# Performance work log

Measured on AMD Instinct MI355X. Metric: run time of the kernel, lower is better.

The kernel has to match this reference:

```python
import jax, jax.numpy as jnp
import numpy as np

N_INP = 512
N_HID = 512
BATCH = 64
STEPS = 512


def setup_inputs() -> dict:
    key = jax.random.key(0)
    ks = jax.random.split(key, 7)

    def xavier(k, n_in, n_out):
        bound = np.sqrt(3.0) * np.sqrt(2.0 / float(n_in + n_out))
        return jax.random.uniform(k, (n_in, n_out), jnp.float32, -bound, bound)

    return {
        "inputs": jax.random.normal(ks[0], (BATCH, STEPS, N_INP), jnp.float32),
        "W_xz": xavier(ks[1], N_INP, N_HID),
        "W_hz": xavier(ks[2], N_HID, N_HID),
        "b_z": jnp.zeros((N_HID,), jnp.float32),
        "W_xr": xavier(ks[3], N_INP, N_HID),
        "W_hr": xavier(ks[4], N_HID, N_HID),
        "b_r": jnp.zeros((N_HID,), jnp.float32),
        "W_xh": xavier(ks[5], N_INP, N_HID),
        "W_hh": xavier(ks[6], N_HID, N_HID),
        "b_h": jnp.zeros((N_HID,), jnp.float32),
        "train": 0,
    }


def reference(inputs, W_xz, W_hz, b_z, W_xr, W_hr, b_r, W_xh, W_hh, b_h, train):
    # inputs: (B, T, n_inp). GRU with eval-mode (dropout_rate=0), so the
    # dropout branch in the original forward is a no-op.
    B = inputs.shape[0]
    H0 = jnp.zeros((B, W_hz.shape[0]), inputs.dtype)

    def step(H_t, X_t):
        Z_t = jax.nn.sigmoid(X_t @ W_xz + H_t @ W_hz + b_z)
        R_t = jax.nn.sigmoid(X_t @ W_xr + H_t @ W_hr + b_r)
        H_tilde = jnp.tanh(X_t @ W_xh + (R_t * H_t) @ W_hh + b_h)
        H_new = Z_t * H_t + (1.0 - Z_t) * H_tilde
        return H_new, H_new

    xs = jnp.swapaxes(inputs, 0, 1)  # (T, B, n_inp)
    H_final, outs = jax.lax.scan(step, H0, xs)
    outputs = jnp.swapaxes(outs, 0, 1)  # (B, T, n_hid)
    return outputs, H_final
```

## Files before the change

### kernel.cpp

```cpp
#include <hip/hip_runtime.h>

#define B_   64
#define T_   512
#define KIN  512
#define NH   512
#define KEFF 3072
#define NBLK 64
#define NTHR 256

typedef __attribute__((ext_vector_type(8))) short short8;
typedef __attribute__((ext_vector_type(4))) float f32x4;
typedef __attribute__((ext_vector_type(4))) unsigned int u32x4;

__device__ __forceinline__ unsigned short f2b(float f) {
    union { float f; unsigned int u; } v; v.f = f;
    unsigned int u = v.u;
    return (unsigned short)((u + 0x7FFFu + ((u >> 16) & 1u)) >> 16);
}
__device__ __forceinline__ float b2f(unsigned short h) {
    union { float f; unsigned int u; } v; v.u = ((unsigned int)h) << 16;
    return v.f;
}

__global__ void prepack(const float* __restrict__ Wxz, const float* __restrict__ Whz,
                        const float* __restrict__ Wxr, const float* __restrict__ Whr,
                        const float* __restrict__ Wxh, const float* __restrict__ Whh,
                        unsigned short* __restrict__ Bzr, unsigned short* __restrict__ Bh) {
    int keff = blockIdx.x * 256 + threadIdx.x;
    int n    = blockIdx.y;
    int seg  = keff >> 9;
    int k    = keff & 511;
    const float* src;
    int c;
    if (n < 512)       { c = n;        src = (seg < 3) ? Whz : Wxz; }
    else if (n < 1024) { c = n - 512;  src = (seg < 3) ? Whr : Wxr; }
    else               { c = n - 1024; src = (seg < 3) ? Whh : Wxh; }
    float w = src[k * NH + c];
    unsigned short hi = f2b(w);
    unsigned short o  = (seg == 2 || seg == 5) ? f2b(w - b2f(hi)) : hi;
    if (n < 1024) Bzr[(size_t)n * KEFF + keff] = o;
    else          Bh[(size_t)(n - 1024) * KEFF + keff] = o;
}

__device__ __forceinline__ unsigned int ald32(const unsigned int* p) {
    return __hip_atomic_load(p, __ATOMIC_RELAXED, __HIP_MEMORY_SCOPE_AGENT);
}
__device__ __forceinline__ unsigned long long ald64(const void* p) {
    return __hip_atomic_load((const unsigned long long*)p, __ATOMIC_RELAXED,
                             __HIP_MEMORY_SCOPE_AGENT);
}
__device__ __forceinline__ void ast32(unsigned int* p, unsigned int v) {
    __hip_atomic_store(p, v, __ATOMIC_RELAXED, __HIP_MEMORY_SCOPE_AGENT);
}
__device__ __forceinline__ void ast64(void* p, unsigned long long v) {
    __hip_atomic_store((unsigned long long*)p, v, __ATOMIC_RELAXED,
                       __HIP_MEMORY_SCOPE_AGENT);
}

__device__ __forceinline__ void flag_wait(const unsigned int* flags,
                                          unsigned int tgt, int lane) {
    while (1) {
        unsigned int v = ald32(flags + lane);
        if (__all((int)(v >= tgt))) break;
    }
    __builtin_amdgcn_sched_barrier(0);
}

__device__ __forceinline__ int hp_idx(int m, int c) {
    return m * 512 + (c ^ ((m & 7) << 2));
}

__device__ __forceinline__ void cvt_x8(const float* xr, int kp, short8* ahi, short8* alo) {
    f32x4 x0 = *(const f32x4*)(xr + kp);
    f32x4 x1 = *(const f32x4*)(xr + kp + 4);
#pragma unroll
    for (int i = 0; i < 4; ++i) {
        unsigned short h0 = f2b(x0[i]);
        (*ahi)[i] = (short)h0; (*alo)[i] = (short)f2b(x0[i] - b2f(h0));
        unsigned short h1 = f2b(x1[i]);
        (*ahi)[4 + i] = (short)h1; (*alo)[4 + i] = (short)f2b(x1[i] - b2f(h1));
    }
}

__device__ __forceinline__ void unpackw(u32x4 w0, u32x4 w1, short8* ahi, short8* alo) {
    union { unsigned int u[4]; short8 v; } H, L;
    H.u[0] = __builtin_amdgcn_perm(w0[1], w0[0], 0x05040100u);
    H.u[1] = __builtin_amdgcn_perm(w0[3], w0[2], 0x05040100u);
    H.u[2] = __builtin_amdgcn_perm(w1[1], w1[0], 0x05040100u);
    H.u[3] = __builtin_amdgcn_perm(w1[3], w1[2], 0x05040100u);
    L.u[0] = __builtin_amdgcn_perm(w0[1], w0[0], 0x07060302u);
    L.u[1] = __builtin_amdgcn_perm(w0[3], w0[2], 0x07060302u);
    L.u[2] = __builtin_amdgcn_perm(w1[1], w1[0], 0x07060302u);
    L.u[3] = __builtin_amdgcn_perm(w1[3], w1[2], 0x07060302u);
    *ahi = H.v; *alo = L.v;
}

#define MFMA(a, b, c) __builtin_amdgcn_mfma_f32_16x16x32_bf16((a), (b), (c), 0, 0, 0)

__global__ void __launch_bounds__(NTHR, 1) gru_seq(
    const float* __restrict__ X, const float* __restrict__ bz,
    const float* __restrict__ br, const float* __restrict__ bh,
    float* __restrict__ out, float* __restrict__ Zt,
    unsigned int* __restrict__ HP, unsigned int* __restrict__ RHP,
    const unsigned short* __restrict__ Bzr, const unsigned short* __restrict__ Bh,
    unsigned int* flags) {
    const int blk  = blockIdx.x;
    const int tid  = threadIdx.x;
    const int wv   = tid >> 6;
    const int lane = tid & 63;
    const int fm   = lane & 15;
    const int fkc  = lane >> 4;
    const int fk   = fkc * 8;

    __shared__ unsigned int hbuf[4 * 16 * 512];
    __shared__ float comb[2][256];

    const int m1 = wv * 16 + fm;
    const unsigned short* Bp1 = Bzr + (size_t)(blk * 16 + fm) * KEFF;
    const int c1 = blk * 16 + fm;

    const int mt    = blk & 3;
    const int slot  = wv >> 1;
    const int khalf = wv & 1;
    const int nt    = (blk >> 2) * 2 + slot;
    const int m2    = mt * 16 + fm;
    const unsigned short* Bp2 = Bh + (size_t)(nt * 16 + fm) * KEFF;
    const int c2 = nt * 16 + fm;

    const int key = (fm & 7) << 4;
    const int sw0 = (32 * fkc) ^ key;
    const int sw1 = (32 * fkc + 16) ^ key;

    const char* HPb  = (const char*)HP;
    const char* RHPb = (const char*)RHP;

    for (int t = 0; t < T_; ++t) {
        const unsigned int ep = (unsigned int)t * 2u;
        {
            f32x4 acc = {0.f, 0.f, 0.f, 0.f};
            const float* xr = X + (size_t)m1 * (T_ * KIN) + (size_t)t * KIN;
#pragma unroll 4
            for (int j = 0; j < 16; ++j) {
                int kp = j * 32 + fk;
                short8 xhi, xlo; cvt_x8(xr, kp, &xhi, &xlo);
                short8 b3 = *(const short8*)(Bp1 + 1536 + kp);
                short8 b4 = *(const short8*)(Bp1 + 2048 + kp);
                short8 b5 = *(const short8*)(Bp1 + 2560 + kp);
                acc = MFMA(xhi, b3, acc); acc = MFMA(xlo, b4, acc); acc = MFMA(xhi, b5, acc);
            }
            if (wv == 0 && t) flag_wait(flags, ep, lane);
            __syncthreads();
            {
                const char* src = HPb + wv * 32768;
                char* dst = (char*)hbuf + wv * 32768;
#pragma unroll
                for (int i = 0; i < 32; ++i)
                    __builtin_amdgcn_global_load_lds(
                        (const unsigned int*)(src + i * 1024 + lane * 16),
                        (unsigned int*)(dst + i * 1024), 16, 0, 0x11);
            }
            asm volatile("s_waitcnt vmcnt(0)" ::: "memory");
            __builtin_amdgcn_sched_barrier(0);
            {
                const char* sl = (const char*)hbuf + wv * 32768 + fm * 2048;
#pragma unroll 4
                for (int j = 0; j < 16; ++j) {
                    u32x4 w0 = *(const u32x4*)(sl + 128 * j + sw0);
                    u32x4 w1 = *(const u32x4*)(sl + 128 * j + sw1);
                    short8 ahi, alo; unpackw(w0, w1, &ahi, &alo);
                    int kp = j * 32 + fk;
                    short8 b0 = *(const short8*)(Bp1 + kp);
                    short8 b1 = *(const short8*)(Bp1 + 512 + kp);
                    short8 b2 = *(const short8*)(Bp1 + 1024 + kp);
                    acc = MFMA(ahi, b0, acc); acc = MFMA(alo, b1, acc); acc = MFMA(ahi, b2, acc);
                }
            }
            if (blk < 32) {
                float bzi = bz[c1];
                float g[4];
#pragma unroll
                for (int jj = 0; jj < 4; ++jj)
                    g[jj] = 1.f / (1.f + __expf(-(acc[jj] + bzi)));
                union { float f[2]; unsigned long long q; } p0, p1;
                p0.f[0] = g[0]; p0.f[1] = g[1];
                p1.f[0] = g[2]; p1.f[1] = g[3];
                float* zp = Zt + c1 * 64 + wv * 16 + fkc * 4;
                ast64(zp, p0.q); ast64(zp + 2, p1.q);
            } else {
                int cr = c1 - 512;
                float bri = br[cr];
#pragma unroll
                for (int jj = 0; jj < 4; ++jj) {
                    int lr = fkc * 4 + jj;
                    unsigned int hw = *(const unsigned int*)((const char*)hbuf +
                        wv * 32768 + lr * 2048 + ((4 * cr) ^ ((lr & 7) << 4)));
                    float h  = b2f((unsigned short)(hw & 0xffffu)) +
                               b2f((unsigned short)(hw >> 16));
                    float gr = 1.f / (1.f + __expf(-(acc[jj] + bri)));
                    float rh = gr * h;
                    unsigned short hi = f2b(rh);
                    unsigned short lo = f2b(rh - b2f(hi));
                    ast32(RHP + hp_idx(wv * 16 + lr, cr),
                          (unsigned int)hi | ((unsigned int)lo << 16));
                }
            }
        }
        __syncthreads();
        if (tid == 0) ast32(flags + blk, ep + 1u);
        {
            f32x4 acc2 = {0.f, 0.f, 0.f, 0.f};
            if (khalf == 1) {
                const float* xr = X + (size_t)m2 * (T_ * KIN) + (size_t)t * KIN;
#pragma unroll 4
                for (int j = 0; j < 16; ++j) {
                    int kp = j * 32 + fk;
                    short8 xhi, xlo; cvt_x8(xr, kp, &xhi, &xlo);
                    short8 b3 = *(const short8*)(Bp2 + 1536 + kp);
                    short8 b4 = *(const short8*)(Bp2 + 2048 + kp);
                    short8 b5 = *(const short8*)(Bp2 + 2560 + kp);
                    acc2 = MFMA(xhi, b3, acc2); acc2 = MFMA(xlo, b4, acc2); acc2 = MFMA(xhi, b5, acc2);
                }
#pragma unroll
                for (int jj = 0; jj < 4; ++jj)
                    comb[slot][(fkc * 4 + jj) * 16 + fm] = acc2[jj];
            }
            if (wv == 0) flag_wait(flags, ep + 1u, lane);
            __syncthreads();
            unsigned long long zq0 = 0, zq1 = 0;
            if (khalf == 0) {
                const float* zp = Zt + c2 * 64 + mt * 16 + fkc * 4;
                zq0 = ald64(zp); zq1 = ald64(zp + 2);
            }
            {
                const char* src = RHPb + mt * 32768;
                char* dst = (char*)hbuf + ((mt + 2) & 3) * 32768;
#pragma unroll
                for (int i = 0; i < 8; ++i) {
                    int o = (wv * 8 + i) * 1024;
                    __builtin_amdgcn_global_load_lds(
                        (const unsigned int*)(src + o + lane * 16),
                        (unsigned int*)(dst + o), 16, 0, 0x11);
                }
            }
            asm volatile("s_waitcnt vmcnt(0)" ::: "memory");
            __builtin_amdgcn_sched_barrier(0);
            __syncthreads();
            if (khalf == 0) {
                const char* sl = (const char*)hbuf + ((mt + 2) & 3) * 32768 + fm * 2048;
#pragma unroll 4
                for (int j = 0; j < 16; ++j) {
                    u32x4 w0 = *(const u32x4*)(sl + 128 * j + sw0);
                    u32x4 w1 = *(const u32x4*)(sl + 128 * j + sw1);
                    short8 ahi, alo; unpackw(w0, w1, &ahi, &alo);
                    int kp = j * 32 + fk;
                    short8 b0 = *(const short8*)(Bp2 + kp);
                    short8 b1 = *(const short8*)(Bp2 + 512 + kp);
                    short8 b2 = *(const short8*)(Bp2 + 1024 + kp);
                    acc2 = MFMA(ahi, b0, acc2); acc2 = MFMA(alo, b1, acc2); acc2 = MFMA(ahi, b2, acc2);
                }
                union { unsigned long long q; float f[2]; } z0, z1;
                z0.q = zq0; z1.q = zq1;
                float zv[4] = {z0.f[0], z0.f[1], z1.f[0], z1.f[1]};
                float bhi = bh[c2];
#pragma unroll
                for (int jj = 0; jj < 4; ++jj) {
                    int lr   = fkc * 4 + jj;
                    int mrow = mt * 16 + lr;
                    unsigned int hw = *(const unsigned int*)((const char*)hbuf +
                        mt * 32768 + lr * 2048 + ((4 * c2) ^ ((lr & 7) << 4)));
                    float h   = b2f((unsigned short)(hw & 0xffffu)) +
                                b2f((unsigned short)(hw >> 16));
                    float pre = acc2[jj] + comb[slot][lr * 16 + fm] + bhi;
                    float e   = __expf(-2.f * pre);
                    float ht  = 2.f / (1.f + e) - 1.f;
                    float hn  = zv[jj] * h + (1.f - zv[jj]) * ht;
                    out[(size_t)mrow * (T_ * NH) + (size_t)t * NH + c2] = hn;
                    if (t == T_ - 1)
                        out[(size_t)B_ * T_ * NH + mrow * NH + c2] = hn;
                    unsigned short hi = f2b(hn);
                    unsigned short lo = f2b(hn - b2f(hi));
                    ast32(HP + hp_idx(mrow, c2),
                          (unsigned int)hi | ((unsigned int)lo << 16));
                }
            }
        }
        __syncthreads();
        if (tid == 0) ast32(flags + blk, ep + 2u);
    }
}

extern "C" void kernel_launch(void* const* d_in, const int* in_sizes, int n_in,
                              void* d_out, int out_size, void* d_ws, size_t ws_size,
                              hipStream_t stream) {
    (void)in_sizes; (void)n_in; (void)out_size; (void)ws_size;
    const float* X   = (const float*)d_in[0];
    const float* Wxz = (const float*)d_in[1];
    const float* Whz = (const float*)d_in[2];
    const float* bz  = (const float*)d_in[3];
    const float* Wxr = (const float*)d_in[4];
    const float* Whr = (const float*)d_in[5];
    const float* br  = (const float*)d_in[6];
    const float* Wxh = (const float*)d_in[7];
    const float* Whh = (const float*)d_in[8];
    const float* bh  = (const float*)d_in[9];
    float* out = (float*)d_out;

    char* ws = (char*)d_ws;
    unsigned int* flags = (unsigned int*)ws;
    float* Zt         = (float*)(ws + 256);
    unsigned int* HP  = (unsigned int*)(ws + 256 + 131072);
    unsigned int* RHP = (unsigned int*)(ws + 256 + 262144);
    unsigned short* Bzr = (unsigned short*)(ws + (1 << 20));
    unsigned short* Bh  = Bzr + (size_t)1024 * KEFF;

    hipMemsetAsync(d_ws, 0, 1 << 20, stream);
    prepack<<<dim3(12, 1536), 256, 0, stream>>>(Wxz, Whz, Wxr, Whr, Wxh, Whh, Bzr, Bh);
    gru_seq<<<NBLK, NTHR, 0, stream>>>(X, bz, br, bh, out, Zt, HP, RHP, Bzr, Bh, flags);
}
```

Before: 14.78 ms.

## Add producer warps that precompute next-step input projections, split recurrent K

Doubles the block to 512 threads. Four extra waves (an "x crew") compute the input-side projections X·W for step t+1 into double-buffered shared memory. Meanwhile the original four waves do the recurrent H·W products and gates for step t, which takes the input GEMM off the serial critical path. The candidate-state recurrent matmul is also split across two waves per tile by K halves and combined through shared memory. The cost is more shared memory, extra barriers, and higher register and wave pressure per CU.

```diff
diff --git a/kernel.cpp b/kernel.cpp
--- a/kernel.cpp
+++ b/kernel.cpp
@@ -6,7 +6,7 @@
 #define NH   512
 #define KEFF 3072
 #define NBLK 64
-#define NTHR 256
+#define NTHR 512
 
 typedef __attribute__((ext_vector_type(8))) short short8;
 typedef __attribute__((ext_vector_type(4))) float f32x4;
@@ -97,7 +97,7 @@
 
 #define MFMA(a, b, c) __builtin_amdgcn_mfma_f32_16x16x32_bf16((a), (b), (c), 0, 0, 0)
 
-__global__ void __launch_bounds__(NTHR, 1) gru_seq(
+__global__ void __launch_bounds__(NTHR, 2) gru_seq(
     const float* __restrict__ X, const float* __restrict__ bz,
     const float* __restrict__ br, const float* __restrict__ bh,
     float* __restrict__ out, float* __restrict__ Zt,
@@ -107,181 +107,204 @@
     const int blk  = blockIdx.x;
     const int tid  = threadIdx.x;
     const int wv   = tid >> 6;
+    const int hwv  = wv & 3;
+    const bool xcrew = wv >= 4;
     const int lane = tid & 63;
     const int fm   = lane & 15;
     const int fkc  = lane >> 4;
     const int fk   = fkc * 8;
 
     __shared__ unsigned int hbuf[4 * 16 * 512];
+    __shared__ float xp1[2][4][16][16];
+    __shared__ float xp2a[2][2][16][16];
+    __shared__ float xp2b[2][2][16][16];
     __shared__ float comb[2][256];
 
-    const int m1 = wv * 16 + fm;
+    const int m1 = hwv * 16 + fm;
     const unsigned short* Bp1 = Bzr + (size_t)(blk * 16 + fm) * KEFF;
     const int c1 = blk * 16 + fm;
 
-    const int mt    = blk & 3;
-    const int slot  = wv >> 1;
-    const int khalf = wv & 1;
-    const int nt    = (blk >> 2) * 2 + slot;
-    const int m2    = mt * 16 + fm;
+    const int mt  = blk & 3;
+    const int s2i = hwv >> 1;
+    const int jh  = hwv & 1;
+    const int nt  = (blk >> 2) * 2 + s2i;
+    const int m2  = mt * 16 + fm;
     const unsigned short* Bp2 = Bh + (size_t)(nt * 16 + fm) * KEFF;
     const int c2 = nt * 16 + fm;
 
     const int key = (fm & 7) << 4;
     const int sw0 = (32 * fkc) ^ key;
     const int sw1 = (32 * fkc + 16) ^ key;
-
     const char* HPb  = (const char*)HP;
     const char* RHPb = (const char*)RHP;
 
+    const float bias1 = (blk < 32) ? bz[c1] : br[c1 - 512];
+    const float bhi   = bh[c2];
+
+    auto xg1 = [&](int tt, int buf) {
+        f32x4 acc = {0.f, 0.f, 0.f, 0.f};
+        const float* xr = X + (size_t)m1 * (T_ * KIN) + (size_t)tt * KIN;
+#pragma unroll 4
+        for (int j = 0; j < 16; ++j) {
+            int kp = j * 32 + fk;
+            short8 xhi, xlo; cvt_x8(xr, kp, &xhi, &xlo);
+            short8 b3 = *(const short8*)(Bp1 + 1536 + kp);
+            short8 b4 = *(const short8*)(Bp1 + 2048 + kp);
+            short8 b5 = *(const short8*)(Bp1 + 2560 + kp);
+            acc = MFMA(xhi, b3, acc); acc = MFMA(xlo, b4, acc); acc = MFMA(xhi, b5, acc);
+        }
+#pragma unroll
+        for (int jj = 0; jj < 4; ++jj) xp1[buf][hwv][fkc * 4 + jj][fm] = acc[jj];
+    };
+    auto xg2 = [&](int tt, int buf) {
+        f32x4 acc = {0.f, 0.f, 0.f, 0.f};
+        const float* xr = X + (size_t)m2 * (T_ * KIN) + (size_t)tt * KIN;
+#pragma unroll
+        for (int j = jh * 8; j < jh * 8 + 8; ++j) {
+            int kp = j * 32 + fk;
+            short8 xhi, xlo; cvt_x8(xr, kp, &xhi, &xlo);
+            short8 b3 = *(const short8*)(Bp2 + 1536 + kp);
+            short8 b4 = *(const short8*)(Bp2 + 2048 + kp);
+            short8 b5 = *(const short8*)(Bp2 + 2560 + kp);
+            acc = MFMA(xhi, b3, acc); acc = MFMA(xlo, b4, acc); acc = MFMA(xhi, b5, acc);
+        }
+        float (*dst)[16][16] = jh ? xp2b[buf] : xp2a[buf];
+#pragma unroll
+        for (int jj = 0; jj < 4; ++jj) dst[s2i][fkc * 4 + jj][fm] = acc[jj];
+    };
+
+    if (xcrew) { xg1(0, 0); xg2(0, 0); }
+    __syncthreads();
+
     for (int t = 0; t < T_; ++t) {
+        const int bufc = t & 1, bufn = bufc ^ 1;
         const unsigned int ep = (unsigned int)t * 2u;
-        {
+        if (wv == 0 && t) flag_wait(flags, ep, lane);
+        __syncthreads();
+        if (!xcrew) {
+            const char* src = HPb + hwv * 32768;
+            char* dst = (char*)hbuf + hwv * 32768;
+#pragma unroll
+            for (int i = 0; i < 32; ++i)
+                __builtin_amdgcn_global_load_lds(
+                    (const unsigned int*)(src + i * 1024 + lane * 16),
+                    (unsigned int*)(dst + i * 1024), 16, 0, 0x11);
+            asm volatile("s_waitcnt vmcnt(0)" ::: "memory");
+            __builtin_amdgcn_sched_barrier(0);
             f32x4 acc = {0.f, 0.f, 0.f, 0.f};
-            const float* xr = X + (size_t)m1 * (T_ * KIN) + (size_t)t * KIN;
+            const char* sl = (const char*)hbuf + hwv * 32768 + fm * 2048;
 #pragma unroll 4
             for (int j = 0; j < 16; ++j) {
+                u32x4 w0 = *(const u32x4*)(sl + 128 * j + sw0);
+                u32x4 w1 = *(const u32x4*)(sl + 128 * j + sw1);
+                short8 ahi, alo; unpackw(w0, w1, &ahi, &alo);
                 int kp = j * 32 + fk;
-                short8 xhi, xlo; cvt_x8(xr, kp, &xhi, &xlo);
-                short8 b3 = *(const short8*)(Bp1 + 1536 + kp);
-                short8 b4 = *(const short8*)(Bp1 + 2048 + kp);
-                short8 b5 = *(const short8*)(Bp1 + 2560 + kp);
-                acc = MFMA(xhi, b3, acc); acc = MFMA(xlo, b4, acc); acc = MFMA(xhi, b5, acc);
-            }
-            if (wv == 0 && t) flag_wait(flags, ep, lane);
-            __syncthreads();
-            {
-                const char* src = HPb + wv * 32768;
-                char* dst = (char*)hbuf + wv * 32768;
-#pragma unroll
-                for (int i = 0; i < 32; ++i)
-                    __builtin_amdgcn_global_load_lds(
-                        (const unsigned int*)(src + i * 1024 + lane * 16),
-                        (unsigned int*)(dst + i * 1024), 16, 0, 0x11);
-            }
-            asm volatile("s_waitcnt vmcnt(0)" ::: "memory");
-            __builtin_amdgcn_sched_barrier(0);
-            {
-                const char* sl = (const char*)hbuf + wv * 32768 + fm * 2048;
-#pragma unroll 4
-                for (int j = 0; j < 16; ++j) {
-                    u32x4 w0 = *(const u32x4*)(sl + 128 * j + sw0);
-                    u32x4 w1 = *(const u32x4*)(sl + 128 * j + sw1);
-                    short8 ahi, alo; unpackw(w0, w1, &ahi, &alo);
-                    int kp = j * 32 + fk;
-                    short8 b0 = *(const short8*)(Bp1 + kp);
-                    short8 b1 = *(const short8*)(Bp1 + 512 + kp);
-                    short8 b2 = *(const short8*)(Bp1 + 1024 + kp);
-                    acc = MFMA(ahi, b0, acc); acc = MFMA(alo, b1, acc); acc = MFMA(ahi, b2, acc);
-                }
+                short8 b0 = *(const short8*)(Bp1 + kp);
+                short8 b1 = *(const short8*)(Bp1 + 512 + kp);
+                short8 b2 = *(const short8*)(Bp1 + 1024 + kp);
+                acc = MFMA(ahi, b0, acc); acc = MFMA(alo, b1, acc); acc = MFMA(ahi, b2, acc);
             }
             if (blk < 32) {
-                float bzi = bz[c1];
                 float g[4];
 #pragma unroll
                 for (int jj = 0; jj < 4; ++jj)
-                    g[jj] = 1.f / (1.f + __expf(-(acc[jj] + bzi)));
+                    g[jj] = 1.f / (1.f + __expf(-(acc[jj] +
+                              xp1[bufc][hwv][fkc * 4 + jj][fm] + bias1)));
                 union { float f[2]; unsigned long long q; } p0, p1;
                 p0.f[0] = g[0]; p0.f[1] = g[1];
                 p1.f[0] = g[2]; p1.f[1] = g[3];
-                float* zp = Zt + c1 * 64 + wv * 16 + fkc * 4;
+                float* zp = Zt + c1 * 64 + hwv * 16 + fkc * 4;
                 ast64(zp, p0.q); ast64(zp + 2, p1.q);
             } else {
                 int cr = c1 - 512;
-                float bri = br[cr];
 #pragma unroll
                 for (int jj = 0; jj < 4; ++jj) {
                     int lr = fkc * 4 + jj;
                     unsigned int hw = *(const unsigned int*)((const char*)hbuf +
-                        wv * 32768 + lr * 2048 + ((4 * cr) ^ ((lr & 7) << 4)));
+                        hwv * 32768 + lr * 2048 + ((4 * cr) ^ ((lr & 7) << 4)));
                     float h  = b2f((unsigned short)(hw & 0xffffu)) +
                                b2f((unsigned short)(hw >> 16));
-                    float gr = 1.f / (1.f + __expf(-(acc[jj] + bri)));
+                    float gr = 1.f / (1.f + __expf(-(acc[jj] +
+                                 xp1[bufc][hwv][lr][fm] + bias1)));
                     float rh = gr * h;
                     unsigned short hi = f2b(rh);
                     unsigned short lo = f2b(rh - b2f(hi));
-                    ast32(RHP + hp_idx(wv * 16 + lr, cr),
+                    ast32(RHP + hp_idx(hwv * 16 + lr, cr),
                           (unsigned int)hi | ((unsigned int)lo << 16));
                 }
             }
+        } else if (t + 1 < T_) {
+            xg1(t + 1, bufn);
         }
         __syncthreads();
         if (tid == 0) ast32(flags + blk, ep + 1u);
-        {
-            f32x4 acc2 = {0.f, 0.f, 0.f, 0.f};
-            if (khalf == 1) {
-                const float* xr = X + (size_t)m2 * (T_ * KIN) + (size_t)t * KIN;
-#pragma unroll 4
-                for (int j = 0; j < 16; ++j) {
-                    int kp = j * 32 + fk;
-                    short8 xhi, xlo; cvt_x8(xr, kp, &xhi, &xlo);
-                    short8 b3 = *(const short8*)(Bp2 + 1536 + kp);
-                    short8 b4 = *(const short8*)(Bp2 + 2048 + kp);
-                    short8 b5 = *(const short8*)(Bp2 + 2560 + kp);
-                    acc2 = MFMA(xhi, b3, acc2); acc2 = MFMA(xlo, b4, acc2); acc2 = MFMA(xhi, b5, acc2);
-                }
-#pragma unroll
-                for (int jj = 0; jj < 4; ++jj)
-                    comb[slot][(fkc * 4 + jj) * 16 + fm] = acc2[jj];
-            }
-            if (wv == 0) flag_wait(flags, ep + 1u, lane);
-            __syncthreads();
-            unsigned long long zq0 = 0, zq1 = 0;
-            if (khalf == 0) {
+        if (wv == 0) flag_wait(flags, ep + 1u, lane);
+        if (xcrew && t + 1 < T_) xg2(t + 1, bufn);
+        __syncthreads();
+        unsigned long long zq0 = 0, zq1 = 0;
+        if (!xcrew) {
+            if (jh == 0) {
                 const float* zp = Zt + c2 * 64 + mt * 16 + fkc * 4;
                 zq0 = ald64(zp); zq1 = ald64(zp + 2);
             }
-            {
-                const char* src = RHPb + mt * 32768;
-                char* dst = (char*)hbuf + ((mt + 2) & 3) * 32768;
-#pragma unroll
-                for (int i = 0; i < 8; ++i) {
-                    int o = (wv * 8 + i) * 1024;
-                    __builtin_amdgcn_global_load_lds(
-                        (const unsigned int*)(src + o + lane * 16),
-                        (unsigned int*)(dst + o), 16, 0, 0x11);
-                }
+            const char* srcR = RHPb + mt * 32768;
+            char* dstR = (char*)hbuf + ((mt + 2) & 3) * 32768;
+#pragma unroll
+            for (int i = 0; i < 8; ++i) {
+                int o = (hwv * 8 + i) * 1024;
+                __builtin_amdgcn_global_load_lds(
+                    (const unsigned int*)(srcR + o + lane * 16),
+                    (unsigned int*)(dstR + o), 16, 0, 0x11);
             }
             asm volatile("s_waitcnt vmcnt(0)" ::: "memory");
             __builtin_amdgcn_sched_barrier(0);
-            __syncthreads();
-            if (khalf == 0) {
-                const char* sl = (const char*)hbuf + ((mt + 2) & 3) * 32768 + fm * 2048;
-#pragma unroll 4
-                for (int j = 0; j < 16; ++j) {
-                    u32x4 w0 = *(const u32x4*)(sl + 128 * j + sw0);
-                    u32x4 w1 = *(const u32x4*)(sl + 128 * j + sw1);
-                    short8 ahi, alo; unpackw(w0, w1, &ahi, &alo);
-                    int kp = j * 32 + fk;
-                    short8 b0 = *(const short8*)(Bp2 + kp);
-                    short8 b1 = *(const short8*)(Bp2 + 512 + kp);
-                    short8 b2 = *(const short8*)(Bp2 + 1024 + kp);
-                    acc2 = MFMA(ahi, b0, acc2); acc2 = MFMA(alo, b1, acc2); acc2 = MFMA(ahi, b2, acc2);
-                }
-                union { unsigned long long q; float f[2]; } z0, z1;
-                z0.q = zq0; z1.q = zq1;
-                float zv[4] = {z0.f[0], z0.f[1], z1.f[0], z1.f[1]};
-                float bhi = bh[c2];
-#pragma unroll
-                for (int jj = 0; jj < 4; ++jj) {
-                    int lr   = fkc * 4 + jj;
-                    int mrow = mt * 16 + lr;
-                    unsigned int hw = *(const unsigned int*)((const char*)hbuf +
-                        mt * 32768 + lr * 2048 + ((4 * c2) ^ ((lr & 7) << 4)));
-                    float h   = b2f((unsigned short)(hw & 0xffffu)) +
-                                b2f((unsigned short)(hw >> 16));
-                    float pre = acc2[jj] + comb[slot][lr * 16 + fm] + bhi;
-                    float e   = __expf(-2.f * pre);
-                    float ht  = 2.f / (1.f + e) - 1.f;
-                    float hn  = zv[jj] * h + (1.f - zv[jj]) * ht;
-                    out[(size_t)mrow * (T_ * NH) + (size_t)t * NH + c2] = hn;
-                    if (t == T_ - 1)
-                        out[(size_t)B_ * T_ * NH + mrow * NH + c2] = hn;
-                    unsigned short hi = f2b(hn);
-                    unsigned short lo = f2b(hn - b2f(hi));
-                    ast32(HP + hp_idx(mrow, c2),
-                          (unsigned int)hi | ((unsigned int)lo << 16));
-                }
+        }
+        __syncthreads();
+        f32x4 acc2 = {0.f, 0.f, 0.f, 0.f};
+        if (!xcrew) {
+            const char* sl2 = (const char*)hbuf + ((mt + 2) & 3) * 32768 + fm * 2048;
+#pragma unroll
+            for (int j = jh * 8; j < jh * 8 + 8; ++j) {
+                u32x4 w0 = *(const u32x4*)(sl2 + 128 * j + sw0);
+                u32x4 w1 = *(const u32x4*)(sl2 + 128 * j + sw1);
+                short8 ahi, alo; unpackw(w0, w1, &ahi, &alo);
+                int kp = j * 32 + fk;
+                short8 b0 = *(const short8*)(Bp2 + kp);
+                short8 b1 = *(const short8*)(Bp2 + 512 + kp);
+                short8 b2 = *(const short8*)(Bp2 + 1024 + kp);
+                acc2 = MFMA(ahi, b0, acc2); acc2 = MFMA(alo, b1, acc2); acc2 = MFMA(ahi, b2, acc2);
+            }
+            if (jh == 1) {
+#pragma unroll
+                for (int jj = 0; jj < 4; ++jj)
+                    comb[s2i][(fkc * 4 + jj) * 16 + fm] = acc2[jj];
+            }
+        }
+        __syncthreads();
+        if (!xcrew && jh == 0) {
+            union { unsigned long long q; float f[2]; } z0, z1;
+            z0.q = zq0; z1.q = zq1;
+            float zv[4] = {z0.f[0], z0.f[1], z1.f[0], z1.f[1]};
+#pragma unroll
+            for (int jj = 0; jj < 4; ++jj) {
+                int lr   = fkc * 4 + jj;
+                int mrow = mt * 16 + lr;
+                unsigned int hw = *(const unsigned int*)((const char*)hbuf +
+                    mt * 32768 + lr * 2048 + ((4 * c2) ^ ((lr & 7) << 4)));
+                float h   = b2f((unsigned short)(hw & 0xffffu)) +
+                            b2f((unsigned short)(hw >> 16));
+                float pre = acc2[jj] + comb[s2i][lr * 16 + fm] +
+                            xp2a[bufc][s2i][lr][fm] + xp2b[bufc][s2i][lr][fm] + bhi;
+                float e   = __expf(-2.f * pre);
+                float ht  = 2.f / (1.f + e) - 1.f;
+                float hn  = zv[jj] * h + (1.f - zv[jj]) * ht;
+                out[(size_t)mrow * (T_ * NH) + (size_t)t * NH + c2] = hn;
+                if (t == T_ - 1)
+                    out[(size_t)B_ * T_ * NH + mrow * NH + c2] = hn;
+                unsigned short hi = f2b(hn);
+                unsigned short lo = f2b(hn - b2f(hi));
+                ast32(HP + hp_idx(mrow, c2),
+                      (unsigned int)hi | ((unsigned int)lo << 16));
             }
         }
         __syncthreads();
```

Result: faster. 14.47 ms (-2.1%).
